# Kernel tuning notes

Hardware: AMD Instinct MI355X
Metric: run time of the kernel (lower is better)

## Reference

```python
import jax, jax.numpy as jnp
import numpy as np

SIGMA = 0.1
B = 1.0
EPS = 1e-5


def setup_inputs() -> dict:
    key = jax.random.key(0)
    k1, k2 = jax.random.split(key)
    featureT = jax.random.normal(k1, (2, 256, 64, 64), dtype=jnp.float32)
    featureI = jax.random.normal(k2, (2, 256, 64, 64), dtype=jnp.float32)
    return {"featureT": featureT, "featureI": featureI}


def reference(featureT, featureI):
    # NCHW -> NHWC
    fI = jnp.transpose(featureI, (0, 2, 3, 1))
    fT = jnp.transpose(featureT, (0, 2, 3, 1))
    # center both by target mean over N, H, W (shape [1,1,1,C])
    meanT = fT.mean(axis=(0, 1, 2), keepdims=True)
    fI = fI - meanT
    fT = fT - meanT
    # channelwise L2 normalize
    fI = fI / jnp.linalg.norm(fI, axis=3, keepdims=True)
    fT = fT / jnp.linalg.norm(fT, axis=3, keepdims=True)
    N, H, W, C = fT.shape
    P = H * W
    # conv2d with 1x1 target patches == cosine similarity vs every target patch
    Tp = fT.reshape(N, P, C)                       # [N, P, C]
    dist = jnp.einsum('nhwc,npc->nhwp', fI, Tp)    # [N, H, W, P]
    raw_dist = (1.0 - dist) / 2.0
    # relative distance: divide by min over target-patch axis
    rel = raw_dist / (jnp.min(raw_dist, axis=3, keepdims=True) + EPS)
    # exp weighting, normalized over target-patch axis
    Wt = jnp.exp((B - rel) / SIGMA)
    CX = Wt / Wt.sum(axis=3, keepdims=True)        # [N, H, W, P]
    # max over spatial (query) dims, mean over target patches, -log, mean
    CX = CX.max(axis=2).max(axis=1)                # [N, P]
    CX = -jnp.log(CX.mean(axis=1))                 # [N]
    return jnp.mean(CX)
```

## Files before the change

### kernel.cpp

```cpp
#include <hip/hip_runtime.h>
#include <hip/hip_bf16.h>
#include <math.h>

#define NB 2
#define C 256
#define P 4096
#define EPS_F 1e-5f

typedef __attribute__((ext_vector_type(8))) short short8;
typedef __attribute__((ext_vector_type(4))) float f32x4;

__device__ __forceinline__ float bf2f(unsigned short u) {
    union { unsigned int i; float f; } x;
    x.i = ((unsigned int)u) << 16;
    return x.f;
}

__global__ void k_mean(const float* __restrict__ fT, float* __restrict__ mean) {
    int c = blockIdx.x;
    int t = threadIdx.x;
    const float* p0 = fT + (size_t)c * P;
    const float* p1 = fT + (size_t)(C + c) * P;
    float s = 0.f;
    for (int i = t; i < P; i += 256) s += p0[i] + p1[i];
    __shared__ float red[256];
    red[t] = s; __syncthreads();
    for (int o = 128; o > 0; o >>= 1) { if (t < o) red[t] += red[t + o]; __syncthreads(); }
    if (t == 0) mean[c] = red[0] * (1.f / 8192.f);
}

__global__ __launch_bounds__(256) void k_normpack(const float* __restrict__ f,
                                                  const float* __restrict__ mean,
                                                  __hip_bfloat16* __restrict__ out) {
    __shared__ float mn[C];
    __shared__ float tile[C][33];
    __shared__ float part[8][32];
    __shared__ float srn[32];
    int t = threadIdx.x;
    mn[t] = mean[t];
    __syncthreads();
    int n = blockIdx.y, p0 = blockIdx.x * 32;
    int pl = t & 31, cg = t >> 5;
    const float* base = f + (size_t)n * C * P + p0 + pl;
    float acc = 0.f;
    #pragma unroll 4
    for (int cc = 0; cc < 32; cc++) {
        int c = cg * 32 + cc;
        float v = base[(size_t)c * P] - mn[c];
        tile[c][pl] = v;
        acc += v * v;
    }
    part[cg][pl] = acc;
    __syncthreads();
    if (t < 32) {
        float s = 0.f;
        #pragma unroll
        for (int g = 0; g < 8; g++) s += part[g][t];
        srn[t] = rsqrtf(s);
    }
    __syncthreads();
    #pragma unroll
    for (int it = 0; it < 4; it++) {
        int flat = it * 2048 + t * 8;
        int p = flat >> 8;
        int c = flat & 255;
        float rn = srn[p];
        union { __hip_bfloat16 h[8]; short8 s; } u;
        #pragma unroll
        for (int k = 0; k < 8; k++)
            u.h[k] = __float2bfloat16(tile[c + k][p] * rn);
        *(short8*)(out + ((size_t)(n * P + p0 + p)) * C + c) = u.s;
    }
}

__device__ __forceinline__ void stage_tile(const __hip_bfloat16* __restrict__ gbase,
                                           __hip_bfloat16* lbuf, int kk, int wid, int lane) {
    #pragma unroll
    for (int j = 0; j < 2; j++) {
        int row = wid * 32 + j * 16 + (lane >> 2);
        int cb = (lane & 3) * 16;
        int scb = cb ^ (((row >> 1) & 3) << 4);
        const char* gp = (const char*)gbase + (size_t)row * (C * 2) + kk * 64 + scb;
        char* lp = (char*)lbuf + (wid * 32 + j * 16) * 64;
        __builtin_amdgcn_global_load_lds(
            (const __attribute__((address_space(1))) void*)gp,
            (__attribute__((address_space(3))) void*)lp, 16, 0, 0);
    }
}

__device__ __forceinline__ short8 ldfrag(const __hip_bfloat16* lbuf, int rloc, int kb) {
    int addr = rloc * 64 + (kb ^ (((rloc >> 1) & 3) << 4));
    return *(const short8*)((const char*)lbuf + addr);
}

__global__ __launch_bounds__(256) void k_gemm(const __hip_bfloat16* __restrict__ TI,
                                              const __hip_bfloat16* __restrict__ TT,
                                              __hip_bfloat16* __restrict__ D,
                                              float* __restrict__ Mpart) {
    __shared__ __hip_bfloat16 lA[2][128 * 32];
    __shared__ __hip_bfloat16 lB[2][128 * 32];
    int lane = threadIdx.x & 63, wid = threadIdx.x >> 6;
    int wr = wid >> 1, wc = wid & 1;
    int n = blockIdx.z;
    int i = blockIdx.x;
    int swz = (i & 7) * 128 + (i >> 3);
    int by = swz >> 5, bx = swz & 31;
    const __hip_bfloat16* A = TI + ((size_t)n * P + by * 128) * C;
    const __hip_bfloat16* B = TT + ((size_t)n * P + bx * 128) * C;

    f32x4 acc[4][4];
    #pragma unroll
    for (int m = 0; m < 4; m++)
        #pragma unroll
        for (int nt = 0; nt < 4; nt++)
            acc[m][nt] = (f32x4){0.f, 0.f, 0.f, 0.f};

    int rA = lane & 15;
    int kb = (lane >> 4) * 16;

    stage_tile(A, lA[0], 0, wid, lane);
    stage_tile(B, lB[0], 0, wid, lane);
    __syncthreads();

    #pragma unroll
    for (int t = 0; t < 8; t++) {
        int cur = t & 1;
        if (t < 7) {
            stage_tile(A, lA[cur ^ 1], t + 1, wid, lane);
            stage_tile(B, lB[cur ^ 1], t + 1, wid, lane);
        }
        short8 a[4], b[4];
        #pragma unroll
        for (int m = 0; m < 4; m++)
            a[m] = ldfrag(lA[cur], wr * 64 + m * 16 + rA, kb);
        #pragma unroll
        for (int nt = 0; nt < 4; nt++)
            b[nt] = ldfrag(lB[cur], wc * 64 + nt * 16 + rA, kb);
        #pragma unroll
        for (int m = 0; m < 4; m++)
            #pragma unroll
            for (int nt = 0; nt < 4; nt++)
                acc[m][nt] = __builtin_amdgcn_mfma_f32_16x16x32_bf16(a[m], b[nt], acc[m][nt], 0, 0, 0);
        __syncthreads();
    }

    int qb = by * 128 + wr * 64;
    int pb = bx * 128 + wc * 64;
    int rj = (lane >> 4) * 4, cl = lane & 15;
    __hip_bfloat16* Dn = D + (size_t)n * P * P;
    #pragma unroll
    for (int m = 0; m < 4; m++)
        #pragma unroll
        for (int nt = 0; nt < 4; nt++)
            #pragma unroll
            for (int j = 0; j < 4; j++)
                Dn[(size_t)(qb + m * 16 + rj + j) * P + pb + nt * 16 + cl] =
                    __float2bfloat16(acc[m][nt][j]);

    int pt = bx * 2 + wc;
    #pragma unroll
    for (int m = 0; m < 4; m++) {
        f32x4 mx = acc[m][0];
        #pragma unroll
        for (int nt = 1; nt < 4; nt++)
            #pragma unroll
            for (int j = 0; j < 4; j++)
                mx[j] = fmaxf(mx[j], acc[m][nt][j]);
        #pragma unroll
        for (int j = 0; j < 4; j++)
            #pragma unroll
            for (int o = 1; o < 16; o <<= 1)
                mx[j] = fmaxf(mx[j], __shfl_xor(mx[j], o));
        if ((lane & 15) == 0) {
            int qbase = qb + m * 16 + (lane >> 4) * 4;
            #pragma unroll
            for (int j = 0; j < 4; j++)
                Mpart[((size_t)(n * P + qbase + j)) * 64 + pt] = mx[j];
        }
    }
}

__global__ __launch_bounds__(256) void k_rowz(const __hip_bfloat16* __restrict__ D,
                                              const float* __restrict__ Mpart,
                                              float* __restrict__ t2a,
                                              float* __restrict__ ca) {
    int row = blockIdx.x;
    int t = threadIdx.x, lane = t & 63, w = t >> 6;
    float m = Mpart[(size_t)row * 64 + lane];
    #pragma unroll
    for (int o = 32; o > 0; o >>= 1) m = fmaxf(m, __shfl_xor(m, o));
    float t2 = 5.f / ((1.f - m) * 0.5f + EPS_F);
    const short8* src = (const short8*)(D + (size_t)row * P);
    float z = 0.f;
    #pragma unroll
    for (int i = 0; i < 2; i++) {
        short8 v = src[t + 256 * i];
        #pragma unroll
        for (int j = 0; j < 8; j++)
            z += __expf(t2 * (bf2f((unsigned short)v[j]) - m));
    }
    #pragma unroll
    for (int o = 32; o > 0; o >>= 1) z += __shfl_xor(z, o);
    __shared__ float redz[4];
    if (lane == 0) redz[w] = z;
    __syncthreads();
    if (t == 0) {
        float zz = redz[0] + redz[1] + redz[2] + redz[3];
        t2a[row] = t2;
        ca[row] = -t2 * m - logf(zz);
    }
}

__global__ __launch_bounds__(256) void k_colmax(const __hip_bfloat16* __restrict__ D,
                                                const float* __restrict__ t2a,
                                                const float* __restrict__ ca,
                                                float* __restrict__ Cpart) {
    __shared__ float st2[64], sc[64];
    int t = threadIdx.x, lane = t & 63, w = t >> 6;
    int n = blockIdx.z, q0 = blockIdx.y * 64;
    int p0 = blockIdx.x * 512 + lane * 8;
    if (t < 64) {
        st2[t] = t2a[n * P + q0 + t];
        sc[t]  = ca[n * P + q0 + t];
    }
    __syncthreads();
    float cmax[8];
    #pragma unroll
    for (int j = 0; j < 8; j++) cmax[j] = -1e30f;
    const char* base = (const char*)(D + ((size_t)n * P + q0) * P + p0);
    #pragma unroll 4
    for (int it = 0; it < 16; it++) {
        int r = it * 4 + w;
        short8 v = *(const short8*)(base + (size_t)r * (P * 2));
        float tt = st2[r], cc = sc[r];
        #pragma unroll
        for (int j = 0; j < 8; j++)
            cmax[j] = fmaxf(cmax[j], fmaf(tt, bf2f((unsigned short)v[j]), cc));
    }
    __shared__ float cred[4][512];
    #pragma unroll
    for (int j = 0; j < 8; j++) cred[w][lane * 8 + j] = cmax[j];
    __syncthreads();
    {
        float* cp = Cpart + ((size_t)(n * 64 + blockIdx.y)) * P + blockIdx.x * 512;
        #pragma unroll
        for (int i = 0; i < 2; i++) {
            int c = t + 256 * i;
            float m0 = fmaxf(fmaxf(cred[0][c], cred[1][c]), fmaxf(cred[2][c], cred[3][c]));
            cp[c] = m0;
        }
    }
}

__global__ void k_colred(const float* __restrict__ Cpart, float* __restrict__ colmax) {
    int np = blockIdx.x * 256 + threadIdx.x;
    int n = np >> 12, p = np & 4095;
    float c = -1e30f;
    for (int g = 0; g < 64; g++)
        c = fmaxf(c, Cpart[((size_t)(n * 64 + g)) * P + p]);
    colmax[np] = __expf(c);
}

__global__ void k_final(const float* __restrict__ colmax, float* __restrict__ out) {
    __shared__ float red[256];
    int t = threadIdx.x;
    float cx[NB];
    for (int n = 0; n < NB; n++) {
        float s = 0.f;
        for (int i = t; i < P; i += 256) s += colmax[n * P + i];
        red[t] = s; __syncthreads();
        for (int o = 128; o > 0; o >>= 1) { if (t < o) red[t] += red[t + o]; __syncthreads(); }
        cx[n] = -logf(red[0] * (1.f / (float)P));
        __syncthreads();
    }
    if (t == 0) out[0] = 0.5f * (cx[0] + cx[1]);
}

extern "C" void kernel_launch(void* const* d_in, const int* in_sizes, int n_in,
                              void* d_out, int out_size, void* d_ws, size_t ws_size,
                              hipStream_t stream) {
    const float* fT = (const float*)d_in[0];
    const float* fI = (const float*)d_in[1];
    float* out = (float*)d_out;

    char* ws = (char*)d_ws;
    size_t off = 0;
    __hip_bfloat16* TI = (__hip_bfloat16*)(ws + off); off += 4194304;
    __hip_bfloat16* TT = (__hip_bfloat16*)(ws + off); off += 4194304;
    __hip_bfloat16* D  = (__hip_bfloat16*)(ws + off); off += (size_t)NB * P * P * 2;
    float* Mpart  = (float*)(ws + off); off += (size_t)NB * P * 64 * 4;
    float* Cpart  = (float*)(ws + off); off += (size_t)NB * 64 * P * 4;
    float* mean   = (float*)(ws + off); off += 1024;
    float* t2a    = (float*)(ws + off); off += 32768;
    float* ca     = (float*)(ws + off); off += 32768;
    float* colmax = (float*)(ws + off); off += 32768;

    k_mean<<<256, 256, 0, stream>>>(fT, mean);
    k_normpack<<<dim3(128, 2), 256, 0, stream>>>(fI, mean, TI);
    k_normpack<<<dim3(128, 2), 256, 0, stream>>>(fT, mean, TT);
    k_gemm<<<dim3(1024, 1, 2), 256, 0, stream>>>(TI, TT, D, Mpart);
    k_rowz<<<8192, 256, 0, stream>>>(D, Mpart, t2a, ca);
    k_colmax<<<dim3(8, 64, 2), 256, 0, stream>>>(D, t2a, ca, Cpart);
    k_colred<<<32, 256, 0, stream>>>(Cpart, colmax);
    k_final<<<1, 256, 0, stream>>>(colmax, out);
}
```

Measured before the change: 105.6 us.

## Fuse row softmax normalizer and column max into one kernel

```diff
diff --git a/kernel.cpp b/kernel.cpp
--- a/kernel.cpp
+++ b/kernel.cpp
@@ -15,6 +15,8 @@
     x.i = ((unsigned int)u) << 16;
     return x.f;
 }
+
+#define SWZ(c) ((c) ^ ((((c) >> 3) & 7) << 2))
 
 __global__ void k_mean(const float* __restrict__ fT, float* __restrict__ mean) {
     int c = blockIdx.x;
@@ -102,11 +104,8 @@
     int lane = threadIdx.x & 63, wid = threadIdx.x >> 6;
     int wr = wid >> 1, wc = wid & 1;
     int n = blockIdx.z;
-    int i = blockIdx.x;
-    int swz = (i & 7) * 128 + (i >> 3);
-    int by = swz >> 5, bx = swz & 31;
-    const __hip_bfloat16* A = TI + ((size_t)n * P + by * 128) * C;
-    const __hip_bfloat16* B = TT + ((size_t)n * P + bx * 128) * C;
+    const __hip_bfloat16* A = TI + ((size_t)n * P + blockIdx.y * 128) * C;
+    const __hip_bfloat16* B = TT + ((size_t)n * P + blockIdx.x * 128) * C;
 
     f32x4 acc[4][4];
     #pragma unroll
@@ -144,8 +143,8 @@
         __syncthreads();
     }
 
-    int qb = by * 128 + wr * 64;
-    int pb = bx * 128 + wc * 64;
+    int qb = blockIdx.y * 128 + wr * 64;
+    int pb = blockIdx.x * 128 + wc * 64;
     int rj = (lane >> 4) * 4, cl = lane & 15;
     __hip_bfloat16* Dn = D + (size_t)n * P * P;
     #pragma unroll
@@ -157,7 +156,7 @@
                 Dn[(size_t)(qb + m * 16 + rj + j) * P + pb + nt * 16 + cl] =
                     __float2bfloat16(acc[m][nt][j]);
 
-    int pt = bx * 2 + wc;
+    int pt = blockIdx.x * 2 + wc;
     #pragma unroll
     for (int m = 0; m < 4; m++) {
         f32x4 mx = acc[m][0];
@@ -180,74 +179,87 @@
     }
 }
 
-__global__ __launch_bounds__(256) void k_rowz(const __hip_bfloat16* __restrict__ D,
+__global__ __launch_bounds__(512) void k_zcol(const __hip_bfloat16* __restrict__ D,
                                               const float* __restrict__ Mpart,
-                                              float* __restrict__ t2a,
-                                              float* __restrict__ ca) {
-    int row = blockIdx.x;
-    int t = threadIdx.x, lane = t & 63, w = t >> 6;
-    float m = Mpart[(size_t)row * 64 + lane];
-    #pragma unroll
-    for (int o = 32; o > 0; o >>= 1) m = fmaxf(m, __shfl_xor(m, o));
-    float t2 = 5.f / ((1.f - m) * 0.5f + EPS_F);
-    const short8* src = (const short8*)(D + (size_t)row * P);
-    float z = 0.f;
-    #pragma unroll
-    for (int i = 0; i < 2; i++) {
-        short8 v = src[t + 256 * i];
-        #pragma unroll
-        for (int j = 0; j < 8; j++)
-            z += __expf(t2 * (bf2f((unsigned short)v[j]) - m));
-    }
-    #pragma unroll
-    for (int o = 32; o > 0; o >>= 1) z += __shfl_xor(z, o);
-    __shared__ float redz[4];
-    if (lane == 0) redz[w] = z;
-    __syncthreads();
-    if (t == 0) {
-        float zz = redz[0] + redz[1] + redz[2] + redz[3];
-        t2a[row] = t2;
-        ca[row] = -t2 * m - logf(zz);
-    }
-}
-
-__global__ __launch_bounds__(256) void k_colmax(const __hip_bfloat16* __restrict__ D,
-                                                const float* __restrict__ t2a,
-                                                const float* __restrict__ ca,
-                                                float* __restrict__ Cpart) {
-    __shared__ float st2[64], sc[64];
-    int t = threadIdx.x, lane = t & 63, w = t >> 6;
-    int n = blockIdx.z, q0 = blockIdx.y * 64;
-    int p0 = blockIdx.x * 512 + lane * 8;
-    if (t < 64) {
-        st2[t] = t2a[n * P + q0 + t];
-        sc[t]  = ca[n * P + q0 + t];
-    }
-    __syncthreads();
-    float cmax[8];
-    #pragma unroll
-    for (int j = 0; j < 8; j++) cmax[j] = -1e30f;
-    const char* base = (const char*)(D + ((size_t)n * P + q0) * P + p0);
-    #pragma unroll 4
-    for (int it = 0; it < 16; it++) {
-        int r = it * 4 + w;
-        short8 v = *(const short8*)(base + (size_t)r * (P * 2));
-        float tt = st2[r], cc = sc[r];
-        #pragma unroll
-        for (int j = 0; j < 8; j++)
-            cmax[j] = fmaxf(cmax[j], fmaf(tt, bf2f((unsigned short)v[j]), cc));
-    }
-    __shared__ float cred[4][512];
-    #pragma unroll
-    for (int j = 0; j < 8; j++) cred[w][lane * 8 + j] = cmax[j];
+                                              float* __restrict__ Cpart) {
+    __shared__ float red[4 * 4096];
+    int t = threadIdx.x, lane = t & 63, wv = t >> 6;
+    int n = blockIdx.y, bx = blockIdx.x;
+    int q0 = bx * 32;
+    float cmax[64];
+    #pragma unroll
+    for (int i = 0; i < 64; i++) cmax[i] = -1e30f;
+
+    #pragma unroll
+    for (int rr = 0; rr < 4; rr++) {
+        int q = q0 + rr * 8 + wv;
+        size_t row = (size_t)n * P + q;
+        float m = Mpart[row * 64 + lane];
+        #pragma unroll
+        for (int o = 32; o > 0; o >>= 1) m = fmaxf(m, __shfl_xor(m, o));
+        float t2 = 5.f / ((1.f - m) * 0.5f + EPS_F);
+        const short8* src = (const short8*)(D + row * P);
+        float z = 0.f;
+        #pragma unroll
+        for (int k = 0; k < 8; k++) {
+            short8 v = src[k * 64 + lane];
+            #pragma unroll
+            for (int j = 0; j < 8; j++)
+                z += __expf(t2 * (bf2f((unsigned short)v[j]) - m));
+        }
+        #pragma unroll
+        for (int o = 32; o > 0; o >>= 1) z += __shfl_xor(z, o);
+        float c = -t2 * m - logf(z);
+        #pragma unroll
+        for (int k = 0; k < 8; k++) {
+            short8 v = src[k * 64 + lane];
+            #pragma unroll
+            for (int j = 0; j < 8; j++)
+                cmax[k * 8 + j] = fmaxf(cmax[k * 8 + j],
+                                        fmaf(t2, bf2f((unsigned short)v[j]), c));
+        }
+    }
+    if (wv < 4) {
+        #pragma unroll
+        for (int k = 0; k < 8; k++) {
+            int cb = k * 512 + lane * 8;
+            #pragma unroll
+            for (int jq = 0; jq < 2; jq++) {
+                f32x4 vv = { cmax[k*8+jq*4], cmax[k*8+jq*4+1], cmax[k*8+jq*4+2], cmax[k*8+jq*4+3] };
+                *(f32x4*)&red[wv * 4096 + SWZ(cb + jq * 4)] = vv;
+            }
+        }
+    }
+    __syncthreads();
+    if (wv >= 4) {
+        #pragma unroll
+        for (int k = 0; k < 8; k++) {
+            int cb = k * 512 + lane * 8;
+            #pragma unroll
+            for (int jq = 0; jq < 2; jq++) {
+                float* pp = &red[(wv - 4) * 4096 + SWZ(cb + jq * 4)];
+                f32x4 old = *(f32x4*)pp;
+                #pragma unroll
+                for (int j = 0; j < 4; j++)
+                    old[j] = fmaxf(old[j], cmax[k * 8 + jq * 4 + j]);
+                *(f32x4*)pp = old;
+            }
+        }
+    }
     __syncthreads();
     {
-        float* cp = Cpart + ((size_t)(n * 64 + blockIdx.y)) * P + blockIdx.x * 512;
-        #pragma unroll
-        for (int i = 0; i < 2; i++) {
-            int c = t + 256 * i;
-            float m0 = fmaxf(fmaxf(cred[0][c], cred[1][c]), fmaxf(cred[2][c], cred[3][c]));
-            cp[c] = m0;
+        float* cp = Cpart + ((size_t)(n * 128 + bx)) * P + t * 8;
+        #pragma unroll
+        for (int jq = 0; jq < 2; jq++) {
+            int cb = t * 8 + jq * 4;
+            f32x4 m0 = *(const f32x4*)&red[SWZ(cb)];
+            #pragma unroll
+            for (int r = 1; r < 4; r++) {
+                f32x4 mr = *(const f32x4*)&red[r * 4096 + SWZ(cb)];
+                #pragma unroll
+                for (int j = 0; j < 4; j++) m0[j] = fmaxf(m0[j], mr[j]);
+            }
+            *(f32x4*)(cp + jq * 4) = m0;
         }
     }
 }
@@ -256,8 +268,8 @@
     int np = blockIdx.x * 256 + threadIdx.x;
     int n = np >> 12, p = np & 4095;
     float c = -1e30f;
-    for (int g = 0; g < 64; g++)
-        c = fmaxf(c, Cpart[((size_t)(n * 64 + g)) * P + p]);
+    for (int g = 0; g < 128; g++)
+        c = fmaxf(c, Cpart[((size_t)(n * 128 + g)) * P + p]);
     colmax[np] = __expf(c);
 }
 
@@ -289,18 +301,15 @@
     __hip_bfloat16* TT = (__hip_bfloat16*)(ws + off); off += 4194304;
     __hip_bfloat16* D  = (__hip_bfloat16*)(ws + off); off += (size_t)NB * P * P * 2;
     float* Mpart  = (float*)(ws + off); off += (size_t)NB * P * 64 * 4;
-    float* Cpart  = (float*)(ws + off); off += (size_t)NB * 64 * P * 4;
+    float* Cpart  = (float*)(ws + off); off += (size_t)NB * 128 * P * 4;
     float* mean   = (float*)(ws + off); off += 1024;
-    float* t2a    = (float*)(ws + off); off += 32768;
-    float* ca     = (float*)(ws + off); off += 32768;
     float* colmax = (float*)(ws + off); off += 32768;
 
     k_mean<<<256, 256, 0, stream>>>(fT, mean);
     k_normpack<<<dim3(128, 2), 256, 0, stream>>>(fI, mean, TI);
     k_normpack<<<dim3(128, 2), 256, 0, stream>>>(fT, mean, TT);
-    k_gemm<<<dim3(1024, 1, 2), 256, 0, stream>>>(TI, TT, D, Mpart);
-    k_rowz<<<8192, 256, 0, stream>>>(D, Mpart, t2a, ca);
-    k_colmax<<<dim3(8, 64, 2), 256, 0, stream>>>(D, t2a, ca, Cpart);
+    k_gemm<<<dim3(32, 32, 2), 256, 0, stream>>>(TI, TT, D, Mpart);
+    k_zcol<<<dim3(128, 2), 512, 0, stream>>>(D, Mpart, Cpart);
     k_colred<<<32, 256, 0, stream>>>(Cpart, colmax);
     k_final<<<1, 256, 0, stream>>>(colmax, out);
 }
```

Result: slower. 108.3 us (+2.6%).
